# Kernel optimization log

Hardware: AMD Instinct MI355X
Metric: run time of the kernel (lower is better)

## Reference

```python
import math
import jax, jax.numpy as jnp
import numpy as np

B, T, D, NH = 4, 2048, 1024, 16
HS = D // NH
N_BUCKETS = 32
MAX_DIST = 128


def _relative_position_bucket(rp):
    # bidirectional T5 bucketing, n_buckets=32, max_distance=128
    nb = N_BUCKETS // 2  # 16
    buckets = (rp > 0).astype(jnp.int32) * nb
    rp = jnp.abs(rp)
    max_exact = nb // 2  # 8
    is_small = rp < max_exact
    me = max_exact - 1   # 7
    nbm = nb - 1         # 15
    rp_safe = jnp.maximum(rp, 1).astype(jnp.float32)
    rp_large = me + (jnp.log(rp_safe / me) / math.log(MAX_DIST / me) * (nbm - me)).astype(jnp.int32)
    rp_large = jnp.minimum(rp_large, nbm)
    buckets = buckets + jnp.where(is_small, rp, rp_large)
    return buckets


def compute_bias(rel_emb, qT, kT):
    ctx = jnp.arange(qT, dtype=jnp.int32)[:, None]
    mem = jnp.arange(kT, dtype=jnp.int32)[None, :]
    bucket = _relative_position_bucket(mem - ctx)  # [qT, kT]
    values = rel_emb[bucket]                        # [qT, kT, NH]
    return jnp.transpose(values, (2, 0, 1))[None]   # [1, NH, qT, kT]


def setup_inputs() -> dict:
    key = jax.random.key(0)
    ks = jax.random.split(key, 6)
    s = 0.02
    return {
        "queries": jax.random.normal(ks[0], (B, T, D), jnp.float32),
        "Wq": jax.random.normal(ks[1], (D, D), jnp.float32) * s,
        "Wk": jax.random.normal(ks[2], (D, D), jnp.float32) * s,
        "Wv": jax.random.normal(ks[3], (D, D), jnp.float32) * s,
        "Wo": jax.random.normal(ks[4], (D, D), jnp.float32) * s,
        "rel_emb": jax.random.normal(ks[5], (N_BUCKETS, NH), jnp.float32) * s,
    }


def reference(queries, Wq, Wk, Wv, Wo, rel_emb):
    b, t, d = queries.shape
    def split_heads(x):
        return jnp.transpose(x.reshape(b, t, NH, HS), (0, 2, 1, 3))  # [B, nh, T, hs]
    q = split_heads(queries @ Wq.T)
    k = split_heads(queries @ Wk.T)
    v = split_heads(queries @ Wv.T)
    att = jnp.einsum('bhqd,bhkd->bhqk', q, k) * (1.0 / math.sqrt(HS))
    att = att + compute_bias(rel_emb, t, t)
    att = jax.nn.softmax(att, axis=-1)
    o = jnp.einsum('bhqk,bhkd->bhqd', att, v)
    o = jnp.transpose(o, (0, 2, 1, 3)).reshape(b, t, d)
    return o @ Wo.T
```

## Files before the change

kernel.cpp:

```cpp
#include <hip/hip_runtime.h>
#include <math.h>

#define T_SEQ 2048
#define D_MODEL 1024
#define NHEADS 16
#define HSZ 64
#define BATCH 4

typedef __bf16 bf16x8 __attribute__((ext_vector_type(8)));
typedef __bf16 bf16x4 __attribute__((ext_vector_type(4)));
typedef short short4v __attribute__((ext_vector_type(4)));
typedef float f32x4 __attribute__((ext_vector_type(4)));

__device__ __forceinline__ unsigned short f2bf(float f) {
    unsigned int u = __builtin_bit_cast(unsigned int, f);
    u += 0x7fff + ((u >> 16) & 1);
    return (unsigned short)(u >> 16);
}

__device__ __forceinline__ unsigned int pk2bf(float a, float b) {
#if __has_builtin(__builtin_amdgcn_cvt_pk_bf16_f32)
    typedef __bf16 bf16x2_t __attribute__((ext_vector_type(2)));
    bf16x2_t v = __builtin_amdgcn_cvt_pk_bf16_f32(a, b);
    return __builtin_bit_cast(unsigned int, v);
#else
    return (unsigned int)f2bf(a) | ((unsigned int)f2bf(b) << 16);
#endif
}

__device__ __forceinline__ float fexp2(float x) {
#if __has_builtin(__builtin_amdgcn_exp2f)
    return __builtin_amdgcn_exp2f(x);
#else
    return __builtin_exp2f(x);
#endif
}

__device__ __forceinline__ f32x4 mfma16_bf16(short4v a, short4v b, f32x4 c) {
#if __has_builtin(__builtin_amdgcn_mfma_f32_16x16x16_bf16)
    return __builtin_amdgcn_mfma_f32_16x16x16_bf16(
        __builtin_bit_cast(bf16x4, a), __builtin_bit_cast(bf16x4, b), c, 0, 0, 0);
#elif __has_builtin(__builtin_amdgcn_mfma_f32_16x16x16bf16_1k)
    return __builtin_amdgcn_mfma_f32_16x16x16bf16_1k(a, b, c, 0, 0, 0);
#else
    f32x4 d = c;
    asm volatile("v_mfma_f32_16x16x16_bf16 %0, %1, %2, %0"
                 : "+v"(d) : "v"(a), "v"(b));
    return d;
#endif
}

__device__ __forceinline__ void gld_lds16(const void* g, void* lds) {
    __builtin_amdgcn_global_load_lds(
        (const __attribute__((address_space(1))) unsigned int*)g,
        (__attribute__((address_space(3))) unsigned int*)lds, 16, 0, 0);
}

__device__ __forceinline__ bf16x8 ld8(const unsigned short* p) {
    return *(const bf16x8*)p;
}

__device__ __forceinline__ float t5_bias(int delta, int h, const float* __restrict__ rel) {
    int bucket = delta > 0 ? 16 : 0;
    int arp = delta < 0 ? -delta : delta;
    if (arp < 8) {
        bucket += arp;
    } else {
        float f = logf((float)arp / 7.0f) * (8.0f / logf(128.0f / 7.0f));
        int rl = 7 + (int)f;
        bucket += rl < 15 ? rl : 15;
    }
    return rel[bucket * NHEADS + h] * 1.4426950408889634f;
}

__global__ void prep(const float* __restrict__ x,
                     const float* __restrict__ w0, const float* __restrict__ w1,
                     const float* __restrict__ w2, const float* __restrict__ w3,
                     unsigned short* __restrict__ Xbf,
                     unsigned short* __restrict__ Wbf) {
    int bid = blockIdx.x;
    int tid = threadIdx.x;
    if (bid < 8192) {
        int i = bid * 256 + tid;
        float4 v = ((const float4*)x)[i];
        ushort4 o;
        o.x = f2bf(v.x); o.y = f2bf(v.y); o.z = f2bf(v.z); o.w = f2bf(v.w);
        ((ushort4*)Xbf)[i] = o;
    } else {
        int wsel = (bid - 8192) >> 10;
        const float* srcs[4] = {w0, w1, w2, w3};
        int i = ((bid - 8192) & 1023) * 256 + tid;
        float4 v = ((const float4*)srcs[wsel])[i];
        ushort4 o;
        o.x = f2bf(v.x); o.y = f2bf(v.y); o.z = f2bf(v.z); o.w = f2bf(v.w);
        ((ushort4*)(Wbf + (size_t)wsel * 1048576))[i] = o;
    }
}

template<int MODE>
__global__ __launch_bounds__(256, 2) void gemm_bt(
    const unsigned short* __restrict__ A,
    const unsigned short* __restrict__ Bw,
    void* __restrict__ out)
{
    constexpr int K = 1024;
    __shared__ __align__(16) char smem[36864];
    unsigned short* As = (unsigned short*)smem;
    unsigned short* Bs = (unsigned short*)(smem + 16384);

    const int tid  = threadIdx.x;
    const int wave = tid >> 6;
    const int lane = tid & 63;
    const int quad = lane >> 4;
    const int l16  = lane & 15;
    const int wm   = wave >> 1;
    const int wn   = wave & 1;
    const int bn   = blockIdx.x;
    const int bm   = blockIdx.y;

    const int r_in = lane >> 3;
    const int lc   = (lane & 7) ^ r_in;

    f32x4 acc[4][4];
    #pragma unroll
    for (int m = 0; m < 4; ++m)
        #pragma unroll
        for (int n = 0; n < 4; ++n)
            acc[m][n] = f32x4{0.f, 0.f, 0.f, 0.f};

    const long a_row0 = (long)bm * 128;
    const long b_row0 = (long)bn * 128;

    for (int kt = 0; kt < K / 64; ++kt) {
        __syncthreads();
        const int k0 = kt * 64 + lc * 8;
        #pragma unroll
        for (int c = 0; c < 4; ++c) {
            int cc = wave * 4 + c;
            int r  = cc * 8 + r_in;
            gld_lds16(A  + (a_row0 + r) * K + k0, &As[cc * 512]);
            gld_lds16(Bw + (b_row0 + r) * K + k0, &Bs[cc * 512]);
        }
        __syncthreads();

        bf16x8 af[4][2], bf[4][2];
        #pragma unroll
        for (int m = 0; m < 4; ++m)
            #pragma unroll
            for (int ks = 0; ks < 2; ++ks) {
                int r  = wm * 64 + m * 16 + l16;
                int pc = (ks * 4 + quad) ^ (r & 7);
                af[m][ks] = ld8(&As[r * 64 + pc * 8]);
            }
        #pragma unroll
        for (int n = 0; n < 4; ++n)
            #pragma unroll
            for (int ks = 0; ks < 2; ++ks) {
                int r  = wn * 64 + n * 16 + l16;
                int pc = (ks * 4 + quad) ^ (r & 7);
                bf[n][ks] = ld8(&Bs[r * 64 + pc * 8]);
            }
        #pragma unroll
        for (int ks = 0; ks < 2; ++ks)
            #pragma unroll
            for (int m = 0; m < 4; ++m)
                #pragma unroll
                for (int n = 0; n < 4; ++n)
                    acc[m][n] = __builtin_amdgcn_mfma_f32_16x16x32_bf16(
                        af[m][ks], bf[n][ks], acc[m][n], 0, 0, 0);
    }

    const int which = (MODE == 4) ? (bn >> 3) : 0;
    if (MODE == 3) {
        float* O = (float*)out;
        #pragma unroll
        for (int m = 0; m < 4; ++m) {
            int row = bm * 128 + wm * 64 + m * 16 + quad * 4;
            #pragma unroll
            for (int n = 0; n < 4; ++n) {
                int col = bn * 128 + wn * 64 + n * 16 + l16;
                #pragma unroll
                for (int r = 0; r < 4; ++r)
                    O[(long)(row + r) * 1024 + col] = acc[m][n][r];
            }
        }
    } else if (which == 2) {
        unsigned short* O = (unsigned short*)out + (size_t)2 * 8388608;
        #pragma unroll
        for (int m = 0; m < 4; ++m) {
            int row = bm * 128 + wm * 64 + m * 16 + quad * 4;
            int b = row >> 11, t = row & 2047;
            #pragma unroll
            for (int n = 0; n < 4; ++n) {
                int cl = (bn * 128 + wn * 64 + n * 16 + l16) & 1023;
                int h = cl >> 6, hs = cl & 63;
                ushort4 pk;
                pk.x = f2bf(acc[m][n][0]); pk.y = f2bf(acc[m][n][1]);
                pk.z = f2bf(acc[m][n][2]); pk.w = f2bf(acc[m][n][3]);
                *(ushort4*)&O[(long)((b * 16 + h) * 64 + hs) * 2048 + t] = pk;
            }
        }
    } else {
        __syncthreads();
        unsigned short* Ew = (unsigned short*)smem + wave * 4608;
        const float qs = (which == 0) ? 0.125f * 1.4426950408889634f : 1.0f;
        #pragma unroll
        for (int m = 0; m < 4; ++m)
            #pragma unroll
            for (int n = 0; n < 4; ++n)
                #pragma unroll
                for (int r = 0; r < 4; ++r)
                    Ew[(m * 16 + quad * 4 + r) * 72 + n * 16 + l16] =
                        f2bf(acc[m][n][r] * qs);
        asm volatile("s_waitcnt lgkmcnt(0)" ::: "memory");

        const int cl0 = (bn * 128 + wn * 64) & 1023;
        const int h   = cl0 >> 6;
        const int gr0 = bm * 128 + wm * 64;
        const int b   = gr0 >> 11, t0 = gr0 & 2047;
        unsigned short* O = (unsigned short*)out + (size_t)which * 8388608
                          + ((size_t)(b * 16 + h) * 2048 + t0) * 64;
        #pragma unroll
        for (int rr = 0; rr < 8; ++rr) {
            int row   = rr * 8 + (lane >> 3);
            int chunk = lane & 7;
            uint4 v = *(const uint4*)&Ew[row * 72 + chunk * 8];
            *(uint4*)&O[(size_t)row * 64 + chunk * 8] = v;
        }
    }
}

__global__ __launch_bounds__(256, 4) void attn(
    const unsigned short* __restrict__ Q,
    const unsigned short* __restrict__ Kb,
    const unsigned short* __restrict__ Vt,
    const float* __restrict__ rel,
    unsigned short* __restrict__ AO)
{
    __shared__ __align__(16) char smem[33824];
    unsigned short* KsB = (unsigned short*)smem;
    unsigned short* VsB = (unsigned short*)(smem + 16384);
    float*          Bb  = (float*)(smem + 32768);

    const int tid  = threadIdx.x;
    const int wave = tid >> 6;
    const int lane = tid & 63;
    const int quad = lane >> 4;
    const int l16  = lane & 15;

    const int bh = blockIdx.y;
    const int b  = bh >> 4, h = bh & 15;
    const int q0 = blockIdx.x * 128;

    const unsigned short* Qg = Q  + (long)bh * T_SEQ * HSZ;
    const unsigned short* Kg = Kb + (long)bh * T_SEQ * HSZ;
    const unsigned short* Vg = Vt + (long)bh * HSZ * T_SEQ;

    const int r_in = lane >> 3;
    const int lc   = (lane & 7) ^ r_in;

    {
        #pragma unroll
        for (int c = 0; c < 2; ++c) {
            int cc = wave * 2 + c;
            int r  = cc * 8 + r_in;
            gld_lds16(Kg + (long)r * 64 + lc * 8, &KsB[cc * 512]);
            gld_lds16(Vg + (long)r * T_SEQ + lc * 8, &VsB[cc * 512]);
        }
    }

    for (int i = tid; i < 263; i += 256)
        Bb[i] = t5_bias(i - 131, h, rel);

    bf16x8 qf[2][2];
    #pragma unroll
    for (int nt = 0; nt < 2; ++nt)
        #pragma unroll
        for (int ks = 0; ks < 2; ++ks) {
            int t = q0 + wave * 32 + nt * 16 + l16;
            qf[nt][ks] = ld8(&Qg[(long)t * 64 + ks * 32 + quad * 8]);
        }

    f32x4 o[2][4];
    float li[2];
    #pragma unroll
    for (int nq = 0; nq < 2; ++nq)
        #pragma unroll
        for (int nh = 0; nh < 4; ++nh) o[nq][nh] = f32x4{0.f, 0.f, 0.f, 0.f};
    #pragma unroll
    for (int nq = 0; nq < 2; ++nq) li[nq] = 0.0f;

    const float cneg = rel[15 * NHEADS + h] * 1.4426950408889634f;
    const float cpos = rel[31 * NHEADS + h] * 1.4426950408889634f;

    for (int kt = 0; kt < T_SEQ / 64; ++kt) {
        const int cur = kt & 1;
        __syncthreads();

        if (kt + 1 < T_SEQ / 64) {
            unsigned short* Kn = KsB + (cur ^ 1) * 4096;
            unsigned short* Vn = VsB + (cur ^ 1) * 4096;
            #pragma unroll
            for (int c = 0; c < 2; ++c) {
                int cc = wave * 2 + c;
                int r  = cc * 8 + r_in;
                gld_lds16(Kg + (long)((kt + 1) * 64 + r) * 64 + lc * 8, &Kn[cc * 512]);
                gld_lds16(Vg + (long)r * T_SEQ + (kt + 1) * 64 + lc * 8, &Vn[cc * 512]);
            }
        }

        const unsigned short* Ks = KsB + cur * 4096;
        const unsigned short* Vs = VsB + cur * 4096;

        const int lo = kt * 64 - q0 - 127;
        const int hi = kt * 64 + 63 - q0;
        const bool outband = (lo >= 128) || (hi <= -128);
        const float cb = (lo >= 128) ? cpos : cneg;
        const f32x4 cbv = {cb, cb, cb, cb};

        short4v pfrag[4][2];
        #pragma unroll
        for (int kc = 0; kc < 4; ++kc) {
            int rk = kc * 16 + l16;
            bf16x8 kf0 = ld8(&Ks[rk * 64 + ((quad)     ^ (rk & 7)) * 8]);
            bf16x8 kf1 = ld8(&Ks[rk * 64 + ((4 + quad) ^ (rk & 7)) * 8]);
            #pragma unroll
            for (int nq = 0; nq < 2; ++nq) {
                f32x4 c0;
                if (outband) {
                    c0 = cbv;
                } else {
                    int i0 = kt * 64 + kc * 16 + quad * 4
                           - wave * 32 - nq * 16 - l16 - q0 + 131;
                    i0 = i0 < 0 ? 0 : (i0 > 259 ? 259 : i0);
                    c0 = f32x4{Bb[i0], Bb[i0 + 1], Bb[i0 + 2], Bb[i0 + 3]};
                }
                __builtin_amdgcn_s_setprio(1);
                f32x4 s = __builtin_amdgcn_mfma_f32_16x16x32_bf16(kf0, qf[nq][0], c0, 0, 0, 0);
                s = __builtin_amdgcn_mfma_f32_16x16x32_bf16(kf1, qf[nq][1], s, 0, 0, 0);
                __builtin_amdgcn_s_setprio(0);
                float p[4];
                #pragma unroll
                for (int r = 0; r < 4; ++r) p[r] = fexp2(s[r]);
                li[nq] += (p[0] + p[1]) + (p[2] + p[3]);
                uint2 pk = {pk2bf(p[0], p[1]), pk2bf(p[2], p[3])};
                pfrag[kc][nq] = __builtin_bit_cast(short4v, pk);
            }
        }

        #pragma unroll
        for (int kc = 0; kc < 4; ++kc) {
            short4v vf[4];
            #pragma unroll
            for (int nh = 0; nh < 4; ++nh) {
                int rv = nh * 16 + l16;
                int ch = (kc * 2 + (quad >> 1)) ^ (rv & 7);
                vf[nh] = *(const short4v*)&Vs[rv * 64 + ch * 8 + (quad & 1) * 4];
            }
            __builtin_amdgcn_s_setprio(1);
            #pragma unroll
            for (int nq = 0; nq < 2; ++nq)
                #pragma unroll
                for (int nh = 0; nh < 4; ++nh)
                    o[nq][nh] = mfma16_bf16(pfrag[kc][nq], vf[nh], o[nq][nh]);
            __builtin_amdgcn_s_setprio(0);
        }
    }

    #pragma unroll
    for (int nq = 0; nq < 2; ++nq) {
        li[nq] += __shfl_xor(li[nq], 16);
        li[nq] += __shfl_xor(li[nq], 32);
    }
    float inv[2];
    #pragma unroll
    for (int nq = 0; nq < 2; ++nq) inv[nq] = 1.0f / li[nq];

    #pragma unroll
    for (int nq = 0; nq < 2; ++nq) {
        float iv[4];
        #pragma unroll
        for (int r = 0; r < 4; ++r) iv[r] = __shfl(inv[nq], quad * 4 + r);
        int qrow = q0 + wave * 32 + nq * 16 + quad * 4;
        #pragma unroll
        for (int r = 0; r < 4; ++r)
            #pragma unroll
            for (int nh = 0; nh < 4; ++nh)
                AO[(long)(b * T_SEQ + qrow + r) * D_MODEL + h * 64 + nh * 16 + l16] =
                    f2bf(o[nq][nh][r] * iv[r]);
    }
}

extern "C" void kernel_launch(void* const* d_in, const int* in_sizes, int n_in,
                              void* d_out, int out_size, void* d_ws, size_t ws_size,
                              hipStream_t stream) {
    const float* x   = (const float*)d_in[0];
    const float* wq  = (const float*)d_in[1];
    const float* wk  = (const float*)d_in[2];
    const float* wv  = (const float*)d_in[3];
    const float* wo  = (const float*)d_in[4];
    const float* rel = (const float*)d_in[5];

    char* ws = (char*)d_ws;
    unsigned short* Xbf = (unsigned short*)(ws);
    unsigned short* Wbf = (unsigned short*)(ws + (16l << 20));
    unsigned short* Qb  = (unsigned short*)(ws + (24l << 20));

    prep<<<12288, 256, 0, stream>>>(x, wq, wk, wv, wo, Xbf, Wbf);

    gemm_bt<4><<<dim3(24, 64), 256, 0, stream>>>(Xbf, Wbf, Qb);

    unsigned short* Kbf = Qb + 8388608;
    unsigned short* Vtb = Qb + 16777216;
    unsigned short* AO  = Xbf;
    attn<<<dim3(16, 64), 256, 0, stream>>>(Qb, Kbf, Vtb, rel, AO);

    gemm_bt<3><<<dim3(8, 64), 256, 0, stream>>>(AO, Wbf + 3 * 1048576, d_out);
}
```

Before: 296.2 us.

## Switch attention inner loop to 32x32x16 bf16 MFMA tiles

Rewrites the attention kernel so each wave computes its 32-query tile with 32x32x16 MFMAs for both QK^T and PV instead of 16x16 MFMAs, reshuffling the P fragment across half-waves with lane shuffles. Bias loading, softmax sum and output writeback are adapted to the new 32x32 accumulator layout. Launch bounds change too: occupancy hint goes to 3 for both the GEMM and attention kernels. Larger MFMAs cut instruction count and LDS fragment reads, at the cost of extra cross-lane shuffles and higher register pressure.

```diff
diff --git a/kernel.cpp b/kernel.cpp
--- a/kernel.cpp
+++ b/kernel.cpp
@@ -11,6 +11,7 @@
 typedef __bf16 bf16x4 __attribute__((ext_vector_type(4)));
 typedef short short4v __attribute__((ext_vector_type(4)));
 typedef float f32x4 __attribute__((ext_vector_type(4)));
+typedef float f32x16 __attribute__((ext_vector_type(16)));
 
 __device__ __forceinline__ unsigned short f2bf(float f) {
     unsigned int u = __builtin_bit_cast(unsigned int, f);
@@ -33,20 +34,6 @@
     return __builtin_amdgcn_exp2f(x);
 #else
     return __builtin_exp2f(x);
-#endif
-}
-
-__device__ __forceinline__ f32x4 mfma16_bf16(short4v a, short4v b, f32x4 c) {
-#if __has_builtin(__builtin_amdgcn_mfma_f32_16x16x16_bf16)
-    return __builtin_amdgcn_mfma_f32_16x16x16_bf16(
-        __builtin_bit_cast(bf16x4, a), __builtin_bit_cast(bf16x4, b), c, 0, 0, 0);
-#elif __has_builtin(__builtin_amdgcn_mfma_f32_16x16x16bf16_1k)
-    return __builtin_amdgcn_mfma_f32_16x16x16bf16_1k(a, b, c, 0, 0, 0);
-#else
-    f32x4 d = c;
-    asm volatile("v_mfma_f32_16x16x16_bf16 %0, %1, %2, %0"
-                 : "+v"(d) : "v"(a), "v"(b));
-    return d;
 #endif
 }
 
@@ -98,7 +85,7 @@
 }
 
 template<int MODE>
-__global__ __launch_bounds__(256, 2) void gemm_bt(
+__global__ __launch_bounds__(256, 3) void gemm_bt(
     const unsigned short* __restrict__ A,
     const unsigned short* __restrict__ Bw,
     void* __restrict__ out)
@@ -230,7 +217,7 @@
     }
 }
 
-__global__ __launch_bounds__(256, 4) void attn(
+__global__ __launch_bounds__(256, 3) void attn(
     const unsigned short* __restrict__ Q,
     const unsigned short* __restrict__ Kb,
     const unsigned short* __restrict__ Vt,
@@ -245,8 +232,8 @@
     const int tid  = threadIdx.x;
     const int wave = tid >> 6;
     const int lane = tid & 63;
-    const int quad = lane >> 4;
-    const int l16  = lane & 15;
+    const int l31  = lane & 31;
+    const int h5   = lane >> 5;
 
     const int bh = blockIdx.y;
     const int b  = bh >> 4, h = bh & 15;
@@ -272,23 +259,15 @@
     for (int i = tid; i < 263; i += 256)
         Bb[i] = t5_bias(i - 131, h, rel);
 
-    bf16x8 qf[2][2];
+    const int qrow_lane = q0 + wave * 32 + l31;
+    bf16x8 qf[4];
     #pragma unroll
-    for (int nt = 0; nt < 2; ++nt)
-        #pragma unroll
-        for (int ks = 0; ks < 2; ++ks) {
-            int t = q0 + wave * 32 + nt * 16 + l16;
-            qf[nt][ks] = ld8(&Qg[(long)t * 64 + ks * 32 + quad * 8]);
-        }
-
-    f32x4 o[2][4];
-    float li[2];
-    #pragma unroll
-    for (int nq = 0; nq < 2; ++nq)
-        #pragma unroll
-        for (int nh = 0; nh < 4; ++nh) o[nq][nh] = f32x4{0.f, 0.f, 0.f, 0.f};
-    #pragma unroll
-    for (int nq = 0; nq < 2; ++nq) li[nq] = 0.0f;
+    for (int hsc = 0; hsc < 4; ++hsc)
+        qf[hsc] = ld8(&Qg[(long)qrow_lane * 64 + hsc * 16 + h5 * 8]);
+
+    f32x16 o0 = {0.f,0.f,0.f,0.f,0.f,0.f,0.f,0.f,0.f,0.f,0.f,0.f,0.f,0.f,0.f,0.f};
+    f32x16 o1 = o0;
+    float li = 0.0f;
 
     const float cneg = rel[15 * NHEADS + h] * 1.4426950408889634f;
     const float cpos = rel[31 * NHEADS + h] * 1.4426950408889634f;
@@ -316,78 +295,88 @@
         const int hi = kt * 64 + 63 - q0;
         const bool outband = (lo >= 128) || (hi <= -128);
         const float cb = (lo >= 128) ? cpos : cneg;
-        const f32x4 cbv = {cb, cb, cb, cb};
-
-        short4v pfrag[4][2];
-        #pragma unroll
-        for (int kc = 0; kc < 4; ++kc) {
-            int rk = kc * 16 + l16;
-            bf16x8 kf0 = ld8(&Ks[rk * 64 + ((quad)     ^ (rk & 7)) * 8]);
-            bf16x8 kf1 = ld8(&Ks[rk * 64 + ((4 + quad) ^ (rk & 7)) * 8]);
-            #pragma unroll
-            for (int nq = 0; nq < 2; ++nq) {
-                f32x4 c0;
-                if (outband) {
-                    c0 = cbv;
-                } else {
-                    int i0 = kt * 64 + kc * 16 + quad * 4
-                           - wave * 32 - nq * 16 - l16 - q0 + 131;
+
+        #pragma unroll
+        for (int tt = 0; tt < 2; ++tt) {
+            const int rk = tt * 32 + l31;
+            bf16x8 af[4];
+            #pragma unroll
+            for (int hsc = 0; hsc < 4; ++hsc)
+                af[hsc] = ld8(&Ks[rk * 64 + (((hsc << 1) | h5) ^ (rk & 7)) * 8]);
+
+            f32x16 s;
+            if (outband) {
+                #pragma unroll
+                for (int e = 0; e < 16; ++e) s[e] = cb;
+            } else {
+                const int ibase = kt * 64 + tt * 32 + h5 * 4 + 131 - qrow_lane;
+                #pragma unroll
+                for (int g = 0; g < 4; ++g) {
+                    int i0 = ibase + g * 8;
                     i0 = i0 < 0 ? 0 : (i0 > 259 ? 259 : i0);
-                    c0 = f32x4{Bb[i0], Bb[i0 + 1], Bb[i0 + 2], Bb[i0 + 3]};
+                    #pragma unroll
+                    for (int r = 0; r < 4; ++r) s[g * 4 + r] = Bb[i0 + r];
                 }
+            }
+
+            __builtin_amdgcn_s_setprio(1);
+            #pragma unroll
+            for (int hsc = 0; hsc < 4; ++hsc)
+                s = __builtin_amdgcn_mfma_f32_32x32x16_bf16(af[hsc], qf[hsc], s, 0, 0, 0);
+            __builtin_amdgcn_s_setprio(0);
+
+            float p[16];
+            #pragma unroll
+            for (int e = 0; e < 16; ++e) p[e] = fexp2(s[e]);
+            #pragma unroll
+            for (int e = 0; e < 16; ++e) li += p[e];
+
+            unsigned int x0 = pk2bf(p[0],  p[1]),  x1 = pk2bf(p[2],  p[3]);
+            unsigned int y0 = pk2bf(p[4],  p[5]),  y1 = pk2bf(p[6],  p[7]);
+            unsigned int z0 = pk2bf(p[8],  p[9]),  z1 = pk2bf(p[10], p[11]);
+            unsigned int u0 = pk2bf(p[12], p[13]), u1 = pk2bf(p[14], p[15]);
+            unsigned int sx0 = __shfl_xor((int)x0, 32), sx1 = __shfl_xor((int)x1, 32);
+            unsigned int sy0 = __shfl_xor((int)y0, 32), sy1 = __shfl_xor((int)y1, 32);
+            unsigned int sz0 = __shfl_xor((int)z0, 32), sz1 = __shfl_xor((int)z1, 32);
+            unsigned int su0 = __shfl_xor((int)u0, 32), su1 = __shfl_xor((int)u1, 32);
+            uint4 pw0, pw1;
+            pw0.x = h5 ? sy0 : x0;  pw0.y = h5 ? sy1 : x1;
+            pw0.z = h5 ? y0 : sx0;  pw0.w = h5 ? y1 : sx1;
+            pw1.x = h5 ? su0 : z0;  pw1.y = h5 ? su1 : z1;
+            pw1.z = h5 ? u0 : sz0;  pw1.w = h5 ? u1 : sz1;
+            bf16x8 pf[2] = {__builtin_bit_cast(bf16x8, pw0),
+                            __builtin_bit_cast(bf16x8, pw1)};
+
+            #pragma unroll
+            for (int c = 0; c < 2; ++c) {
+                const int tc = tt * 2 + c;
+                const int rv0 = l31;
+                const int rv1 = 32 + l31;
+                bf16x8 vf0 = ld8(&Vs[rv0 * 64 + (((tc << 1) | h5) ^ (rv0 & 7)) * 8]);
+                bf16x8 vf1 = ld8(&Vs[rv1 * 64 + (((tc << 1) | h5) ^ (rv1 & 7)) * 8]);
                 __builtin_amdgcn_s_setprio(1);
-                f32x4 s = __builtin_amdgcn_mfma_f32_16x16x32_bf16(kf0, qf[nq][0], c0, 0, 0, 0);
-                s = __builtin_amdgcn_mfma_f32_16x16x32_bf16(kf1, qf[nq][1], s, 0, 0, 0);
+                o0 = __builtin_amdgcn_mfma_f32_32x32x16_bf16(pf[c], vf0, o0, 0, 0, 0);
+                o1 = __builtin_amdgcn_mfma_f32_32x32x16_bf16(pf[c], vf1, o1, 0, 0, 0);
                 __builtin_amdgcn_s_setprio(0);
-                float p[4];
-                #pragma unroll
-                for (int r = 0; r < 4; ++r) p[r] = fexp2(s[r]);
-                li[nq] += (p[0] + p[1]) + (p[2] + p[3]);
-                uint2 pk = {pk2bf(p[0], p[1]), pk2bf(p[2], p[3])};
-                pfrag[kc][nq] = __builtin_bit_cast(short4v, pk);
-            }
-        }
-
-        #pragma unroll
-        for (int kc = 0; kc < 4; ++kc) {
-            short4v vf[4];
-            #pragma unroll
-            for (int nh = 0; nh < 4; ++nh) {
-                int rv = nh * 16 + l16;
-                int ch = (kc * 2 + (quad >> 1)) ^ (rv & 7);
-                vf[nh] = *(const short4v*)&Vs[rv * 64 + ch * 8 + (quad & 1) * 4];
-            }
-            __builtin_amdgcn_s_setprio(1);
-            #pragma unroll
-            for (int nq = 0; nq < 2; ++nq)
-                #pragma unroll
-                for (int nh = 0; nh < 4; ++nh)
-                    o[nq][nh] = mfma16_bf16(pfrag[kc][nq], vf[nh], o[nq][nh]);
-            __builtin_amdgcn_s_setprio(0);
-        }
-    }
+            }
+        }
+    }
+
+    li += __shfl_xor(li, 32);
+    const float inv = 1.0f / li;
 
     #pragma unroll
-    for (int nq = 0; nq < 2; ++nq) {
-        li[nq] += __shfl_xor(li[nq], 16);
-        li[nq] += __shfl_xor(li[nq], 32);
-    }
-    float inv[2];
-    #pragma unroll
-    for (int nq = 0; nq < 2; ++nq) inv[nq] = 1.0f / li[nq];
-
-    #pragma unroll
-    for (int nq = 0; nq < 2; ++nq) {
-        float iv[4];
-        #pragma unroll
-        for (int r = 0; r < 4; ++r) iv[r] = __shfl(inv[nq], quad * 4 + r);
-        int qrow = q0 + wave * 32 + nq * 16 + quad * 4;
-        #pragma unroll
-        for (int r = 0; r < 4; ++r)
-            #pragma unroll
-            for (int nh = 0; nh < 4; ++nh)
-                AO[(long)(b * T_SEQ + qrow + r) * D_MODEL + h * 64 + nh * 16 + l16] =
-                    f2bf(o[nq][nh][r] * iv[r]);
+    for (int g = 0; g < 4; ++g) {
+        #pragma unroll
+        for (int r = 0; r < 4; ++r) {
+            const int ql = g * 8 + h5 * 4 + r;
+            const float iv = __shfl(inv, ql);
+            const int qrow = q0 + wave * 32 + ql;
+            unsigned short* dst =
+                &AO[(long)(b * T_SEQ + qrow) * D_MODEL + h * 64 + l31];
+            dst[0]  = f2bf(o0[g * 4 + r] * iv);
+            dst[32] = f2bf(o1[g * 4 + r] * iv);
+        }
     }
 }
 
```

After: 302.6 us. +2.2%, slower.
